# Kernel optimization log

Measured on AMD Instinct MI355X. Metric: run time of the kernel, lower is better.

The kernel has to match this reference:

```python
import jax, jax.numpy as jnp
import numpy as np

NUM_GRAPHS = 1024


def setup_inputs() -> dict:
    key = jax.random.key(0)
    k1, k2, k3, k4 = jax.random.split(key, 4)
    N, IN, OUT = 500000, 128, 128
    x = jax.random.normal(k1, (N, IN), dtype=jnp.float32)
    batch_id = jnp.sort(jax.random.randint(k2, (N,), 0, NUM_GRAPHS))
    # torch Linear: weight [out_features, in_features_total]
    W = jax.random.normal(k3, (OUT, 2 * IN), dtype=jnp.float32) * (1.0 / np.sqrt(2 * IN))
    b = jax.random.normal(k4, (OUT,), dtype=jnp.float32) * 0.01
    return {"x": x, "batch_id": batch_id, "W": W, "b": b}


def reference(x, batch_id, W, b):
    # global_mean_pool: segment-mean of x over batch_id -> [G, IN]
    sums = jax.ops.segment_sum(x, batch_id, num_segments=NUM_GRAPHS)
    counts = jax.ops.segment_sum(jnp.ones((x.shape[0],), dtype=x.dtype), batch_id,
                                 num_segments=NUM_GRAPHS)
    mean = sums / jnp.maximum(counts, 1.0)[:, None]  # [G, IN]
    # gather per-graph context back to each node, concat, linear
    g_per_node = mean[batch_id]                      # [N, IN]
    inp = jnp.concatenate([x, g_per_node], axis=-1)  # [N, 2*IN]
    return inp @ W.T + b                             # [N, OUT]
```

## Files before the change

### kernel.cpp

```cpp
#include <hip/hip_runtime.h>
#include <hip/hip_bf16.h>


#define G_NUM 1024
#define IN_F 128
#define OUT_F 128

typedef __attribute__((ext_vector_type(8))) short short8;
typedef __attribute__((ext_vector_type(4))) float f32x4;

static __device__ __forceinline__ unsigned short f2bf(float f) {
    union { float f; unsigned u; } v; v.f = f;
    unsigned u = v.u;
    unsigned r = (u + 0x7FFFu + ((u >> 16) & 1u)) >> 16;
    return (unsigned short)r;
}

__global__ void k_wcvt(const float* __restrict__ W, unsigned short* __restrict__ W1b) {
    int i = blockIdx.x * 256 + threadIdx.x;
    if (i < OUT_F * IN_F) {
        int o = i >> 7, k = i & 127;
        W1b[i] = f2bf(W[o * 256 + k]);
    }
}

__global__ __launch_bounds__(256) void k_mean_ctx(
        const float* __restrict__ x, const int* __restrict__ bid,
        const float* __restrict__ W, const float* __restrict__ b,
        float* __restrict__ ctx, int N) {
    int g = blockIdx.x;
    int tid = threadIdx.x;

    int lo = 0, hi = N;
    while (lo < hi) { int m = (lo + hi) >> 1; if (bid[m] < g) lo = m + 1; else hi = m; }
    int start = lo;
    int lo2 = start, hi2 = N;
    while (lo2 < hi2) { int m = (lo2 + hi2) >> 1; if (bid[m] < g + 1) lo2 = m + 1; else hi2 = m; }
    int end = lo2;
    int cnt = end - start;

    __shared__ float4 red[8][32];
    __shared__ float ms[IN_F];

    int c4 = tid & 31;
    int rg = tid >> 5;
    float4 s = make_float4(0.f, 0.f, 0.f, 0.f);
    for (int r = start + rg; r < end; r += 8) {
        float4 v = *(const float4*)(x + (size_t)r * IN_F + c4 * 4);
        s.x += v.x; s.y += v.y; s.z += v.z; s.w += v.w;
    }
    red[rg][c4] = s;
    __syncthreads();
    if (tid < 32) {
        float4 t = red[0][tid];
        #pragma unroll
        for (int i = 1; i < 8; ++i) {
            float4 v = red[i][tid];
            t.x += v.x; t.y += v.y; t.z += v.z; t.w += v.w;
        }
        float inv = 1.0f / (float)(cnt > 0 ? cnt : 1);
        ms[tid * 4 + 0] = t.x * inv;
        ms[tid * 4 + 1] = t.y * inv;
        ms[tid * 4 + 2] = t.z * inv;
        ms[tid * 4 + 3] = t.w * inv;
    }
    __syncthreads();
    if (tid < OUT_F) {
        int o = tid;
        float acc = b[o];
        const float* w2 = W + o * 256 + 128;
        #pragma unroll 8
        for (int k = 0; k < IN_F; ++k) acc += ms[k] * w2[k];
        ctx[g * OUT_F + o] = acc;
    }
}

#define AS_STRIDE 136

__global__ __launch_bounds__(256) void k_gemm(
        const float* __restrict__ x, const int* __restrict__ bid,
        const unsigned short* __restrict__ W1b, const float* __restrict__ ctx,
        float* __restrict__ out, int N) {
    __shared__ unsigned short As[128 * AS_STRIDE];
    __shared__ int bids[128];

    int tid = threadIdx.x;
    int row0 = blockIdx.x * 128;
    int lane = tid & 63, wave = tid >> 6;
    int l16 = lane & 15, quad = lane >> 4;
    int wrow = (wave & 1) * 64;
    int wcol = (wave >> 1) * 64;

    short8 bfrag[4][4];
    #pragma unroll
    for (int ot = 0; ot < 4; ++ot) {
        int o = wcol + ot * 16 + l16;
        #pragma unroll
        for (int kt = 0; kt < 4; ++kt)
            bfrag[kt][ot] = *(const short8*)(W1b + o * IN_F + kt * 32 + quad * 8);
    }

    #pragma unroll
    for (int i = 0; i < 16; ++i) {
        int r = i * 8 + (tid >> 5);
        int c4 = (tid & 31) * 4;
        int gr = row0 + r;
        float4 v = make_float4(0.f, 0.f, 0.f, 0.f);
        if (gr < N) v = *(const float4*)(x + (size_t)gr * IN_F + c4);
        ushort4 p;
        p.x = f2bf(v.x); p.y = f2bf(v.y); p.z = f2bf(v.z); p.w = f2bf(v.w);
        *(ushort4*)&As[r * AS_STRIDE + c4] = p;
    }
    if (tid < 128) bids[tid] = (row0 + tid < N) ? bid[row0 + tid] : 0;
    __syncthreads();

    f32x4 acc[4][4];
    #pragma unroll
    for (int mt = 0; mt < 4; ++mt)
        #pragma unroll
        for (int ot = 0; ot < 4; ++ot)
            acc[mt][ot] = (f32x4){0.f, 0.f, 0.f, 0.f};

    #pragma unroll
    for (int kt = 0; kt < 4; ++kt) {
        short8 af[4];
        #pragma unroll
        for (int mt = 0; mt < 4; ++mt) {
            int m = wrow + mt * 16 + l16;
            af[mt] = *(const short8*)&As[m * AS_STRIDE + kt * 32 + quad * 8];
        }
        #pragma unroll
        for (int mt = 0; mt < 4; ++mt)
            #pragma unroll
            for (int ot = 0; ot < 4; ++ot)
                acc[mt][ot] = __builtin_amdgcn_mfma_f32_16x16x32_bf16(
                    af[mt], bfrag[kt][ot], acc[mt][ot], 0, 0, 0);
    }

    #pragma unroll
    for (int mt = 0; mt < 4; ++mt) {
        #pragma unroll
        for (int r = 0; r < 4; ++r) {
            int row = wrow + mt * 16 + quad * 4 + r;
            int grow = row0 + row;
            if (grow < N) {
                int cb = bids[row] * OUT_F;
                #pragma unroll
                for (int ot = 0; ot < 4; ++ot) {
                    int col = wcol + ot * 16 + l16;
                    out[(size_t)grow * OUT_F + col] = acc[mt][ot][r] + ctx[cb + col];
                }
            }
        }
    }
}

extern "C" void kernel_launch(void* const* d_in, const int* in_sizes, int n_in,
                              void* d_out, int out_size, void* d_ws, size_t ws_size,
                              hipStream_t stream) {
    const float* x  = (const float*)d_in[0];
    const int* bid  = (const int*)d_in[1];
    const float* W  = (const float*)d_in[2];
    const float* b  = (const float*)d_in[3];
    float* out      = (float*)d_out;
    int N = in_sizes[1];

    float* ctx = (float*)d_ws;
    unsigned short* W1b = (unsigned short*)((char*)d_ws + (size_t)G_NUM * OUT_F * sizeof(float));

    k_wcvt<<<(OUT_F * IN_F + 255) / 256, 256, 0, stream>>>(W, W1b);
    k_mean_ctx<<<G_NUM, 256, 0, stream>>>(x, bid, W, b, ctx, N);
    k_gemm<<<(N + 127) / 128, 256, 0, stream>>>(x, bid, W1b, ctx, out, N);
}
```

Baseline: 575.9 us.

## Load GEMM A fragments directly from global, drop LDS staging, unroll mean reduction

The GEMM kernel no longer stages x into shared memory as bf16. Each wave now reads its A fragments straight from global memory per k-tile and converts them in registers, and loads B fragments per k-tile instead of holding them all up front. A fast path adds a single broadcast ctx row when all 128 rows of a block share one graph. The mean kernel's reduction loop is unrolled 4x with independent accumulators to raise memory-level parallelism. The trade-off is that the two column-waves covering the same rows now read those rows from global twice with strided, less coalesced access, in exchange for no LDS, no barrier and higher occupancy.

Result: faster. 547.7 us (-4.9%).

```diff
diff --git a/kernel.cpp b/kernel.cpp
--- a/kernel.cpp
+++ b/kernel.cpp
@@ -14,6 +14,15 @@
     unsigned u = v.u;
     unsigned r = (u + 0x7FFFu + ((u >> 16) & 1u)) >> 16;
     return (unsigned short)r;
+}
+
+static __device__ __forceinline__ short8 pack8(float4 a, float4 b) {
+    short8 o;
+    o[0] = (short)f2bf(a.x); o[1] = (short)f2bf(a.y);
+    o[2] = (short)f2bf(a.z); o[3] = (short)f2bf(a.w);
+    o[4] = (short)f2bf(b.x); o[5] = (short)f2bf(b.y);
+    o[6] = (short)f2bf(b.z); o[7] = (short)f2bf(b.w);
+    return o;
 }
 
 __global__ void k_wcvt(const float* __restrict__ W, unsigned short* __restrict__ W1b) {
@@ -44,12 +53,30 @@
 
     int c4 = tid & 31;
     int rg = tid >> 5;
-    float4 s = make_float4(0.f, 0.f, 0.f, 0.f);
-    for (int r = start + rg; r < end; r += 8) {
-        float4 v = *(const float4*)(x + (size_t)r * IN_F + c4 * 4);
-        s.x += v.x; s.y += v.y; s.z += v.z; s.w += v.w;
-    }
-    red[rg][c4] = s;
+    float4 s0 = make_float4(0.f, 0.f, 0.f, 0.f);
+    float4 s1 = s0, s2 = s0, s3 = s0;
+
+    int r = start + rg;
+    for (; r + 24 < end; r += 32) {
+        float4 a = *(const float4*)(x + (size_t)(r     ) * IN_F + c4 * 4);
+        float4 c = *(const float4*)(x + (size_t)(r +  8) * IN_F + c4 * 4);
+        float4 d = *(const float4*)(x + (size_t)(r + 16) * IN_F + c4 * 4);
+        float4 e = *(const float4*)(x + (size_t)(r + 24) * IN_F + c4 * 4);
+        s0.x += a.x; s0.y += a.y; s0.z += a.z; s0.w += a.w;
+        s1.x += c.x; s1.y += c.y; s1.z += c.z; s1.w += c.w;
+        s2.x += d.x; s2.y += d.y; s2.z += d.z; s2.w += d.w;
+        s3.x += e.x; s3.y += e.y; s3.z += e.z; s3.w += e.w;
+    }
+    for (; r < end; r += 8) {
+        float4 a = *(const float4*)(x + (size_t)r * IN_F + c4 * 4);
+        s0.x += a.x; s0.y += a.y; s0.z += a.z; s0.w += a.w;
+    }
+    s0.x += s1.x + s2.x + s3.x;
+    s0.y += s1.y + s2.y + s3.y;
+    s0.z += s1.z + s2.z + s3.z;
+    s0.w += s1.w + s2.w + s3.w;
+
+    red[rg][c4] = s0;
     __syncthreads();
     if (tid < 32) {
         float4 t = red[0][tid];
@@ -75,15 +102,10 @@
     }
 }
 
-#define AS_STRIDE 136
-
-__global__ __launch_bounds__(256) void k_gemm(
+__global__ __launch_bounds__(256, 2) void k_gemm(
         const float* __restrict__ x, const int* __restrict__ bid,
         const unsigned short* __restrict__ W1b, const float* __restrict__ ctx,
         float* __restrict__ out, int N) {
-    __shared__ unsigned short As[128 * AS_STRIDE];
-    __shared__ int bids[128];
-
     int tid = threadIdx.x;
     int row0 = blockIdx.x * 128;
     int lane = tid & 63, wave = tid >> 6;
@@ -91,29 +113,6 @@
     int wrow = (wave & 1) * 64;
     int wcol = (wave >> 1) * 64;
 
-    short8 bfrag[4][4];
-    #pragma unroll
-    for (int ot = 0; ot < 4; ++ot) {
-        int o = wcol + ot * 16 + l16;
-        #pragma unroll
-        for (int kt = 0; kt < 4; ++kt)
-            bfrag[kt][ot] = *(const short8*)(W1b + o * IN_F + kt * 32 + quad * 8);
-    }
-
-    #pragma unroll
-    for (int i = 0; i < 16; ++i) {
-        int r = i * 8 + (tid >> 5);
-        int c4 = (tid & 31) * 4;
-        int gr = row0 + r;
-        float4 v = make_float4(0.f, 0.f, 0.f, 0.f);
-        if (gr < N) v = *(const float4*)(x + (size_t)gr * IN_F + c4);
-        ushort4 p;
-        p.x = f2bf(v.x); p.y = f2bf(v.y); p.z = f2bf(v.z); p.w = f2bf(v.w);
-        *(ushort4*)&As[r * AS_STRIDE + c4] = p;
-    }
-    if (tid < 128) bids[tid] = (row0 + tid < N) ? bid[row0 + tid] : 0;
-    __syncthreads();
-
     f32x4 acc[4][4];
     #pragma unroll
     for (int mt = 0; mt < 4; ++mt)
@@ -123,32 +122,62 @@
 
     #pragma unroll
     for (int kt = 0; kt < 4; ++kt) {
+        short8 bf[4];
+        #pragma unroll
+        for (int ot = 0; ot < 4; ++ot)
+            bf[ot] = *(const short8*)(W1b + (wcol + ot * 16 + l16) * IN_F + kt * 32 + quad * 8);
         short8 af[4];
         #pragma unroll
         for (int mt = 0; mt < 4; ++mt) {
-            int m = wrow + mt * 16 + l16;
-            af[mt] = *(const short8*)&As[m * AS_STRIDE + kt * 32 + quad * 8];
+            int r = row0 + wrow + mt * 16 + l16;
+            float4 v0 = make_float4(0.f, 0.f, 0.f, 0.f), v1 = v0;
+            if (r < N) {
+                const float* p = x + (size_t)r * IN_F + kt * 32 + quad * 8;
+                v0 = *(const float4*)p;
+                v1 = *(const float4*)(p + 4);
+            }
+            af[mt] = pack8(v0, v1);
         }
         #pragma unroll
         for (int mt = 0; mt < 4; ++mt)
             #pragma unroll
             for (int ot = 0; ot < 4; ++ot)
                 acc[mt][ot] = __builtin_amdgcn_mfma_f32_16x16x32_bf16(
-                    af[mt], bfrag[kt][ot], acc[mt][ot], 0, 0, 0);
-    }
-
-    #pragma unroll
-    for (int mt = 0; mt < 4; ++mt) {
-        #pragma unroll
-        for (int r = 0; r < 4; ++r) {
-            int row = wrow + mt * 16 + quad * 4 + r;
-            int grow = row0 + row;
-            if (grow < N) {
-                int cb = bids[row] * OUT_F;
-                #pragma unroll
-                for (int ot = 0; ot < 4; ++ot) {
-                    int col = wcol + ot * 16 + l16;
-                    out[(size_t)grow * OUT_F + col] = acc[mt][ot][r] + ctx[cb + col];
+                    af[mt], bf[ot], acc[mt][ot], 0, 0, 0);
+    }
+
+    int lastrow = row0 + 127 < N ? row0 + 127 : N - 1;
+    int b_lo = bid[row0], b_hi = bid[lastrow];
+    if (b_lo == b_hi) {
+        float cv[4];
+        #pragma unroll
+        for (int ot = 0; ot < 4; ++ot)
+            cv[ot] = ctx[b_lo * OUT_F + wcol + ot * 16 + l16];
+        #pragma unroll
+        for (int mt = 0; mt < 4; ++mt) {
+            #pragma unroll
+            for (int r4 = 0; r4 < 4; ++r4) {
+                int row = row0 + wrow + mt * 16 + quad * 4 + r4;
+                if (row < N) {
+                    #pragma unroll
+                    for (int ot = 0; ot < 4; ++ot)
+                        out[(size_t)row * OUT_F + wcol + ot * 16 + l16] =
+                            acc[mt][ot][r4] + cv[ot];
+                }
+            }
+        }
+    } else {
+        #pragma unroll
+        for (int mt = 0; mt < 4; ++mt) {
+            #pragma unroll
+            for (int r4 = 0; r4 < 4; ++r4) {
+                int row = row0 + wrow + mt * 16 + quad * 4 + r4;
+                if (row < N) {
+                    int cb = bid[row] * OUT_F;
+                    #pragma unroll
+                    for (int ot = 0; ot < 4; ++ot)
+                        out[(size_t)row * OUT_F + wcol + ot * 16 + l16] =
+                            acc[mt][ot][r4] + ctx[cb + wcol + ot * 16 + l16];
                 }
             }
         }
```
